# Kernel optimization log

Measured on AMD Instinct MI355X. Metric: run time of the kernel, lower is better.

Reference implementation:

```python
import jax, jax.numpy as jnp
import numpy as np

N_HEADS = 8
N_POINTS = 4
SPATIAL = np.array([[64, 64], [32, 32], [16, 16], [8, 8]], dtype=np.int32)


def setup_inputs() -> dict:
    key = jax.random.key(0)
    ks = jax.random.split(key, 12)
    d = 256
    H, L, P, N = N_HEADS, SPATIAL.shape[0], N_POINTS, 8
    lens = SPATIAL[:, 0] * SPATIAL[:, 1]
    Lin = int(lens.sum())
    Lq = Lin
    query = jax.random.normal(ks[0], (N, Lq, d), jnp.float32)
    reference_points = jax.random.uniform(ks[1], (N, Lq, L, 2), jnp.float32)
    input_flatten = jax.random.normal(ks[2], (N, Lin, d), jnp.float32)
    input_spatial_shapes = jnp.asarray(SPATIAL)
    starts = np.concatenate([[0], np.cumsum(lens)[:-1]]).astype(np.int32)
    input_level_start_index = jnp.asarray(starts)
    s = 1.0 / np.sqrt(d)
    W_off = jax.random.normal(ks[3], (H * L * P * 2, d), jnp.float32) * 0.01
    b_off = jax.random.normal(ks[4], (H * L * P * 2,), jnp.float32) * 0.5
    W_attn = jax.random.normal(ks[5], (H * L * P, d), jnp.float32) * 0.02
    b_attn = jnp.zeros((H * L * P,), jnp.float32)
    W_val = jax.random.normal(ks[6], (d, d), jnp.float32) * s
    b_val = jnp.zeros((d,), jnp.float32)
    W_out = jax.random.normal(ks[7], (d, d), jnp.float32) * s
    b_out = jnp.zeros((d,), jnp.float32)
    return {
        'query': query, 'reference_points': reference_points,
        'input_flatten': input_flatten,
        'input_spatial_shapes': input_spatial_shapes,
        'input_level_start_index': input_level_start_index,
        'W_off': W_off, 'b_off': b_off, 'W_attn': W_attn, 'b_attn': b_attn,
        'W_val': W_val, 'b_val': b_val, 'W_out': W_out, 'b_out': b_out,
    }


def _bilinear(img, Hl, Wl, x, y):
    # img: [B, Ch, Hl*Wl]; x, y: [B, Q, P] pixel coords (align_corners=False)
    # zero padding mode: out-of-range corners contribute 0
    x0 = jnp.floor(x)
    y0 = jnp.floor(y)
    wx = x - x0
    wy = y - y0

    def gather(xi, yi):
        valid = (xi >= 0) & (xi <= Wl - 1) & (yi >= 0) & (yi <= Hl - 1)
        ii = jnp.clip(xi, 0, Wl - 1).astype(jnp.int32)
        jj = jnp.clip(yi, 0, Hl - 1).astype(jnp.int32)
        idx = jj * Wl + ii  # [B, Q, P]
        B, Q, P = idx.shape
        v = jnp.take_along_axis(img, idx.reshape(B, 1, Q * P), axis=2)
        v = v.reshape(B, img.shape[1], Q, P)
        return v * valid[:, None].astype(img.dtype)

    return (gather(x0, y0) * ((1 - wx) * (1 - wy))[:, None]
            + gather(x0 + 1, y0) * (wx * (1 - wy))[:, None]
            + gather(x0, y0 + 1) * ((1 - wx) * wy)[:, None]
            + gather(x0 + 1, y0 + 1) * (wx * wy)[:, None])


def reference(query, reference_points, input_flatten, input_spatial_shapes,
              input_level_start_index, W_off, b_off, W_attn, b_attn,
              W_val, b_val, W_out, b_out):
    shapes = np.asarray(input_spatial_shapes)  # static structural metadata
    N, Lq, d = query.shape
    Lin = input_flatten.shape[1]
    L = shapes.shape[0]
    H, P = N_HEADS, N_POINTS
    Ch = d // H

    value = input_flatten @ W_val.T + b_val                       # [N, Lin, d]
    value = value.reshape(N, Lin, H, Ch).transpose(0, 2, 3, 1)    # [N, H, Ch, Lin]
    value = value.reshape(N * H, Ch, Lin)

    off = (query @ W_off.T + b_off).reshape(N, Lq, H, L, P, 2)
    attn = (query @ W_attn.T + b_attn).reshape(N, Lq, H, L * P)
    attn = jax.nn.softmax(attn, axis=-1).reshape(N, Lq, H, L, P)

    # normalizer is (W, H) per level
    norm = jnp.asarray(np.stack([shapes[:, 1], shapes[:, 0]], -1), query.dtype)
    loc = reference_points[:, :, None, :, None, :] + off / norm[None, None, None, :, None, :]

    attn_p = attn.transpose(0, 2, 1, 3, 4).reshape(N * H, Lq, L, P)
    starts = np.concatenate([[0], np.cumsum(shapes[:, 0] * shapes[:, 1])])

    out = jnp.zeros((N * H, Ch, Lq), query.dtype)
    for l in range(L):
        Hl, Wl = int(shapes[l, 0]), int(shapes[l, 1])
        v_l = value[:, :, starts[l]:starts[l + 1]]                # [B, Ch, Hl*Wl]
        g = loc[:, :, :, l].transpose(0, 2, 1, 3, 4).reshape(N * H, Lq, P, 2)
        # grid_sample align_corners=False with grid=2*loc-1 -> pixel = loc*W - 0.5
        x = g[..., 0] * Wl - 0.5
        y = g[..., 1] * Hl - 0.5
        samp = _bilinear(v_l, Hl, Wl, x, y)                       # [B, Ch, Lq, P]
        out = out + jnp.einsum('bcqp,bqp->bcq', samp, attn_p[:, :, l])

    out = out.reshape(N, H, Ch, Lq).transpose(0, 3, 1, 2).reshape(N, Lq, d)
    return out @ W_out.T + b_out
```

## Files before the change

### kernel.cpp

```cpp
#include <hip/hip_runtime.h>
#include <hip/hip_bf16.h>
#include <hip/hip_fp16.h>

#define NQ   5440
#define NB   8
#define DIM  256
#define NH   8
#define CHN  32
#define NLV  4
#define NPT  4
#define MTOT (NB * NQ)

typedef __attribute__((ext_vector_type(8))) short s16x8;
typedef __attribute__((ext_vector_type(4))) float f32x4;
typedef unsigned short ushort_t;
typedef unsigned int uint_t;

#define WVAL 0
#define WOFF 65536
#define WATT 131072
#define WOUT 163840
#define WTOT 229376

__device__ __forceinline__ short f2bf(float x) {
    union { __hip_bfloat16 b; short s; } u;
    u.b = __float2bfloat16(x);
    return u.s;
}

__device__ __forceinline__ void gload_lds16(const void* g, void* l) {
    __builtin_amdgcn_global_load_lds(
        (const __attribute__((address_space(1))) unsigned int*)g,
        (__attribute__((address_space(3))) unsigned int*)l, 16, 0, 0);
}

__device__ __forceinline__ void cvt8b(const float* s, ushort_t* d) {
    f32x4 a = *(const f32x4*)s, b = *(const f32x4*)(s + 4);
    s16x8 v;
#pragma unroll
    for (int e = 0; e < 4; ++e) { v[e] = f2bf(a[e]); v[e + 4] = f2bf(b[e]); }
    *(s16x8*)d = v;
}

__global__ __launch_bounds__(256) void cvt_weights(const float* __restrict__ wv,
                                                   const float* __restrict__ wo,
                                                   const float* __restrict__ wa,
                                                   const float* __restrict__ wu,
                                                   ushort_t* __restrict__ wb) {
    const int i = (blockIdx.x * 256 + threadIdx.x) * 8;
    if (i >= WTOT) return;
    const float* src;
    int off;
    if (i < WOFF)      { src = wv; off = WVAL; }
    else if (i < WATT) { src = wo; off = WOFF; }
    else if (i < WOUT) { src = wa; off = WATT; }
    else               { src = wu; off = WOUT; }
    cvt8b(src + (i - off), wb + i);
}

__device__ __forceinline__ void stC(float* p, float v) { *p = v; }
__device__ __forceinline__ void stC(__half* p, float v) { *p = __float2half(v); }
__device__ __forceinline__ void stC(ushort_t* p, float v) { *(short*)p = f2bf(v); }

template <typename AT, typename CT>
__device__ __forceinline__ void gemm_core(const AT* __restrict__ A,
                                          const ushort_t* __restrict__ Wt,
                                          const float* __restrict__ biasT,
                                          CT* __restrict__ Ct, int ldC, int rowBase) {
    __shared__ ushort_t As[128 * 64];
    __shared__ ushort_t Ws[128 * 64];

    const int t = threadIdx.x;
    const int lane = t & 63, w = t >> 6;
    const int wm = w >> 1, wn = w & 1;
    const int lr = lane & 15, quad = lane >> 4;

    f32x4 acc[4][4];
#pragma unroll
    for (int i = 0; i < 4; ++i)
#pragma unroll
        for (int j = 0; j < 4; ++j)
#pragma unroll
            for (int r = 0; r < 4; ++r) acc[i][j][r] = 0.f;

    for (int ks = 0; ks < 4; ++ks) {
        if (ks) __syncthreads();
#pragma unroll
        for (int i = 0; i < 4; ++i) {
            const int c = t + i * 256;
            const int r = c >> 3, s = c & 7;
            const int g = (s - r) & 7;
            const int ke = ks * 64 + g * 8;
            gload_lds16(Wt + (size_t)r * DIM + ke,
                        &Ws[(size_t)(i * 256 + w * 64) * 8]);
            if constexpr (sizeof(AT) == 2) {
                gload_lds16(A + (size_t)(rowBase + r) * DIM + ke,
                            &As[(size_t)(i * 256 + w * 64) * 8]);
            } else {
                const float* pa = (const float*)A + (size_t)(rowBase + r) * DIM + ke;
                f32x4 a0 = *(const f32x4*)pa, a1 = *(const f32x4*)(pa + 4);
                s16x8 av;
#pragma unroll
                for (int e = 0; e < 4; ++e) {
                    av[e] = f2bf(a0[e]);
                    av[e + 4] = f2bf(a1[e]);
                }
                *(s16x8*)&As[(size_t)c * 8] = av;
            }
        }
        __syncthreads();
#pragma unroll
        for (int kk = 0; kk < 64; kk += 32) {
            s16x8 afr[4], wfr[4];
            const int G = (kk >> 3) + quad;
#pragma unroll
            for (int i = 0; i < 4; ++i) {
                const int R = wm * 64 + i * 16 + lr;
                afr[i] = *(const s16x8*)&As[(R * 8 + ((G + R) & 7)) * 8];
            }
#pragma unroll
            for (int j = 0; j < 4; ++j) {
                const int R = wn * 64 + j * 16 + lr;
                wfr[j] = *(const s16x8*)&Ws[(R * 8 + ((G + R) & 7)) * 8];
            }
#pragma unroll
            for (int i = 0; i < 4; ++i)
#pragma unroll
                for (int j = 0; j < 4; ++j)
                    acc[i][j] = __builtin_amdgcn_mfma_f32_16x16x32_bf16(
                        afr[i], wfr[j], acc[i][j], 0, 0, 0);
        }
    }

    float bj[4];
#pragma unroll
    for (int j = 0; j < 4; ++j) bj[j] = biasT[wn * 64 + j * 16 + lr];
#pragma unroll
    for (int i = 0; i < 4; ++i)
#pragma unroll
        for (int r = 0; r < 4; ++r) {
            int row = rowBase + wm * 64 + i * 16 + quad * 4 + r;
#pragma unroll
            for (int j = 0; j < 4; ++j) {
                int col = wn * 64 + j * 16 + lr;
                stC(&Ct[(size_t)row * ldC + col], acc[i][j][r] + bj[j]);
            }
        }
}

__global__ __launch_bounds__(256) void gemm_fused(const float* __restrict__ inputf,
                                                  const float* __restrict__ query,
                                                  const ushort_t* __restrict__ wb,
                                                  const float* __restrict__ b_val,
                                                  const float* __restrict__ b_off,
                                                  const float* __restrict__ b_attn,
                                                  __half* __restrict__ bval,
                                                  __half* __restrict__ v_off,
                                                  __half* __restrict__ v_attn) {
    const int gy = blockIdx.y;
    const int rowBase = blockIdx.x * 128;
    if (gy < 2)
        gemm_core<float, __half>(inputf, wb + WVAL + (size_t)gy * 128 * DIM,
                                 b_val + gy * 128, bval + gy * 128, DIM, rowBase);
    else if (gy < 4)
        gemm_core<float, __half>(query, wb + WOFF + (size_t)(gy - 2) * 128 * DIM,
                                 b_off + (gy - 2) * 128, v_off + (gy - 2) * 128, DIM,
                                 rowBase);
    else
        gemm_core<float, __half>(query, wb + WATT, b_attn, v_attn, 128, rowBase);
}

__global__ __launch_bounds__(256) void gemm_out(const ushort_t* __restrict__ A,
                                                const ushort_t* __restrict__ wb,
                                                const float* __restrict__ bias,
                                                float* __restrict__ C) {
    gemm_core<ushort_t, float>(A, wb + WOUT + (size_t)blockIdx.y * 128 * DIM,
                               bias + blockIdx.y * 128, C + blockIdx.y * 128, DIM,
                               blockIdx.x * 128);
}

__global__ __launch_bounds__(256, 8) void sample_kernel(
    const float* __restrict__ refp,
    const __half* __restrict__ off,
    const __half* __restrict__ attn,
    const __half* __restrict__ bval,
    const int* __restrict__ shapes,
    const int* __restrict__ starts,
    ushort_t* __restrict__ sampb)
{
    const int n = blockIdx.x & 7;
    const int qBase = n * NQ + (blockIdx.x >> 3) * 8;
    const int t = threadIdx.x;

    __shared__ __align__(16) uint4 sitem[1024];

#pragma unroll
    for (int it = 0; it < 4; ++it) {
        const int i = t + it * 256;
        const int q8 = i >> 7, hlp = i & 127;
        const int h = hlp >> 4, lp = hlp & 15, l = lp >> 2;
        const int q = qBase + q8;
        const int Wl = shapes[2 * l + 1], Hl = shapes[2 * l];
        const float Wf = (float)Wl, Hf = (float)Hl;
        const float2 rp = *(const float2*)(refp + ((size_t)q * NLV + l) * 2);
        const __half2 oo2 = ((const __half2*)off)[(size_t)q * 128 + h * 16 + lp];
        const float2 oo = __half22float2(oo2);
        const float x = (rp.x + oo.x / Wf) * Wf - 0.5f;
        const float y = (rp.y + oo.y / Hf) * Hf - 0.5f;

        float logit = __half2float(attn[(size_t)q * 128 + h * 16 + lp]);
        float m = logit;
#pragma unroll
        for (int s = 8; s >= 1; s >>= 1) m = fmaxf(m, __shfl_xor(m, s, 16));
        float e = __expf(logit - m);
        float ss = e;
#pragma unroll
        for (int s = 8; s >= 1; s >>= 1) ss += __shfl_xor(ss, s, 16);
        const float aw = e / ss;

        const float xf = floorf(x), yf = floorf(y);
        const int ix = (int)xf, iy = (int)yf;
        const float wx = x - xf, wy = y - yf;
        const int ix1 = ix + 1, iy1 = iy + 1;
        const bool bx0 = (ix >= 0) & (ix < Wl);
        const bool bx1 = (ix1 >= 0) & (ix1 < Wl);
        const bool by0 = (iy >= 0) & (iy < Hl);
        const bool by1 = (iy1 >= 0) & (iy1 < Hl);
        const int cx0 = min(max(ix, 0), Wl - 1), cx1 = min(max(ix1, 0), Wl - 1);
        const int cy0 = min(max(iy, 0), Hl - 1), cy1 = min(max(iy1, 0), Hl - 1);
        const int base = n * NQ + starts[l];

        uint4 item;
        item.x = (uint_t)(base + cy0 * Wl + cx0) << 9;
        const uint_t dx  = (uint_t)(cx1 - cx0) << 9;
        const uint_t dyW = (uint_t)((cy1 - cy0) * Wl) << 9;
        item.y = dx | (dyW << 16);
        union { __half2 h; uint_t u; } p01, p23;
        p01.h = __halves2half2(
            __float2half((bx0 && by0) ? aw * (1.f - wx) * (1.f - wy) : 0.f),
            __float2half((bx1 && by0) ? aw * wx * (1.f - wy) : 0.f));
        p23.h = __halves2half2(
            __float2half((bx0 && by1) ? aw * (1.f - wx) * wy : 0.f),
            __float2half((bx1 && by1) ? aw * wx * wy : 0.f));
        item.z = p01.u;
        item.w = p23.u;
        sitem[i] = item;
    }
    __syncthreads();

    const int q8 = t >> 5, r = t & 31;
    const int h = r >> 2, cg = r & 3;
    const int q = qBase + q8;
    const char* vb = (const char*)bval + h * 64 + cg * 16;
    const int slotBase = (q8 << 7) + (h << 4);

    __half2 acch[4];
    float accf[8];
#pragma unroll
    for (int e = 0; e < 4; ++e) acch[e] = __float2half2_rn(0.f);
#pragma unroll
    for (int e = 0; e < 8; ++e) accf[e] = 0.f;

#pragma unroll
    for (int j = 0; j < 16; ++j) {
        const int lp = (j + h) & 15;
        const uint4 itv = sitem[slotBase + lp];
        const uint_t a00 = itv.x;
        const uint_t dx = itv.y & 0xffffu, dyW = itv.y >> 16;
        uint_t ad[4];
        ad[0] = a00;
        ad[1] = a00 + dx;
        ad[2] = a00 + dyW;
        ad[3] = a00 + dx + dyW;
        union { uint_t u; __half2 h; } w01, w23;
        w01.u = itv.z; w23.u = itv.w;
        __half2 wc[4];
        wc[0] = __half2half2(__low2half(w01.h));
        wc[1] = __half2half2(__high2half(w01.h));
        wc[2] = __half2half2(__low2half(w23.h));
        wc[3] = __half2half2(__high2half(w23.h));

        uint4 u[4];
#pragma unroll
        for (int c = 0; c < 4; ++c)
            u[c] = *(const uint4*)(vb + (size_t)ad[c]);
#pragma unroll
        for (int c = 0; c < 4; ++c) {
            const __half2* hv = (const __half2*)&u[c];
#pragma unroll
            for (int e = 0; e < 4; ++e) acch[e] = __hfma2(hv[e], wc[c], acch[e]);
        }
        if ((j & 3) == 3) {
#pragma unroll
            for (int e = 0; e < 4; ++e) {
                float2 f = __half22float2(acch[e]);
                accf[2 * e] += f.x;
                accf[2 * e + 1] += f.y;
                acch[e] = __float2half2_rn(0.f);
            }
        }
    }

    s16x8 o;
#pragma unroll
    for (int e = 0; e < 8; ++e) o[e] = f2bf(accf[e]);
    *(s16x8*)(sampb + (size_t)q * DIM + h * CHN + cg * 8) = o;
}

extern "C" void kernel_launch(void* const* d_in, const int* in_sizes, int n_in,
                              void* d_out, int out_size, void* d_ws, size_t ws_size,
                              hipStream_t stream) {
    const float* query  = (const float*)d_in[0];
    const float* refp   = (const float*)d_in[1];
    const float* inputf = (const float*)d_in[2];
    const int* shapes   = (const int*)d_in[3];
    const int* starts   = (const int*)d_in[4];
    const float* W_off  = (const float*)d_in[5];
    const float* b_off  = (const float*)d_in[6];
    const float* W_attn = (const float*)d_in[7];
    const float* b_attn = (const float*)d_in[8];
    const float* W_val  = (const float*)d_in[9];
    const float* b_val  = (const float*)d_in[10];
    const float* W_out  = (const float*)d_in[11];
    const float* b_out  = (const float*)d_in[12];
    float* out = (float*)d_out;

    const size_t AB = (size_t)MTOT * DIM * 2;
    char* ws = (char*)d_ws;
    ushort_t* wb     = (ushort_t*)ws;
    __half*   bval   = (__half*)(ws + 512 * 1024);
    __half*   v_off  = (__half*)(ws + 512 * 1024 + AB);
    __half*   v_attn = (__half*)(ws + 512 * 1024 + 2 * AB);
    ushort_t* sampb  = (ushort_t*)(ws + 512 * 1024 + 2 * AB + AB / 2);

    cvt_weights<<<dim3(WTOT / 2048), dim3(256), 0, stream>>>(W_val, W_off, W_attn,
                                                             W_out, wb);
    gemm_fused<<<dim3(MTOT / 128, 5), dim3(256), 0, stream>>>(
        inputf, query, wb, b_val, b_off, b_attn, bval, v_off, v_attn);
    sample_kernel<<<dim3(MTOT / 8), dim3(256), 0, stream>>>(
        refp, v_off, v_attn, bval, shapes, starts, sampb);
    gemm_out<<<dim3(MTOT / 128, 2), dim3(256), 0, stream>>>(sampb, wb, b_out, out);
}
```

Before: 275.9 us.

## Fuse deformable sampling with output projection GEMM in one kernel

```diff
diff --git a/kernel.cpp b/kernel.cpp
--- a/kernel.cpp
+++ b/kernel.cpp
@@ -58,15 +58,11 @@
     cvt8b(src + (i - off), wb + i);
 }
 
-__device__ __forceinline__ void stC(float* p, float v) { *p = v; }
-__device__ __forceinline__ void stC(__half* p, float v) { *p = __float2half(v); }
-__device__ __forceinline__ void stC(ushort_t* p, float v) { *(short*)p = f2bf(v); }
-
-template <typename AT, typename CT>
-__device__ __forceinline__ void gemm_core(const AT* __restrict__ A,
-                                          const ushort_t* __restrict__ Wt,
-                                          const float* __restrict__ biasT,
-                                          CT* __restrict__ Ct, int ldC, int rowBase) {
+__device__ __forceinline__ void gemm_core_f32(const float* __restrict__ A,
+                                              const ushort_t* __restrict__ Wt,
+                                              const float* __restrict__ biasT,
+                                              __half* __restrict__ Ct, int ldC,
+                                              int rowBase) {
     __shared__ ushort_t As[128 * 64];
     __shared__ ushort_t Ws[128 * 64];
 
@@ -88,25 +84,20 @@
 #pragma unroll
         for (int i = 0; i < 4; ++i) {
             const int c = t + i * 256;
-            const int r = c >> 3, s = c & 7;
-            const int g = (s - r) & 7;
+            const int r = c >> 3, s2 = c & 7;
+            const int g = (s2 - r) & 7;
             const int ke = ks * 64 + g * 8;
             gload_lds16(Wt + (size_t)r * DIM + ke,
                         &Ws[(size_t)(i * 256 + w * 64) * 8]);
-            if constexpr (sizeof(AT) == 2) {
-                gload_lds16(A + (size_t)(rowBase + r) * DIM + ke,
-                            &As[(size_t)(i * 256 + w * 64) * 8]);
-            } else {
-                const float* pa = (const float*)A + (size_t)(rowBase + r) * DIM + ke;
-                f32x4 a0 = *(const f32x4*)pa, a1 = *(const f32x4*)(pa + 4);
-                s16x8 av;
-#pragma unroll
-                for (int e = 0; e < 4; ++e) {
-                    av[e] = f2bf(a0[e]);
-                    av[e + 4] = f2bf(a1[e]);
-                }
-                *(s16x8*)&As[(size_t)c * 8] = av;
-            }
+            const float* pa = A + (size_t)(rowBase + r) * DIM + ke;
+            f32x4 a0 = *(const f32x4*)pa, a1 = *(const f32x4*)(pa + 4);
+            s16x8 av;
+#pragma unroll
+            for (int e = 0; e < 4; ++e) {
+                av[e] = f2bf(a0[e]);
+                av[e + 4] = f2bf(a1[e]);
+            }
+            *(s16x8*)&As[(size_t)c * 8] = av;
         }
         __syncthreads();
 #pragma unroll
@@ -143,7 +134,7 @@
 #pragma unroll
             for (int j = 0; j < 4; ++j) {
                 int col = wn * 64 + j * 16 + lr;
-                stC(&Ct[(size_t)row * ldC + col], acc[i][j][r] + bj[j]);
+                Ct[(size_t)row * ldC + col] = __float2half(acc[i][j][r] + bj[j]);
             }
         }
 }
@@ -160,151 +151,219 @@
     const int gy = blockIdx.y;
     const int rowBase = blockIdx.x * 128;
     if (gy < 2)
-        gemm_core<float, __half>(inputf, wb + WVAL + (size_t)gy * 128 * DIM,
-                                 b_val + gy * 128, bval + gy * 128, DIM, rowBase);
+        gemm_core_f32(inputf, wb + WVAL + (size_t)gy * 128 * DIM,
+                      b_val + gy * 128, bval + gy * 128, DIM, rowBase);
     else if (gy < 4)
-        gemm_core<float, __half>(query, wb + WOFF + (size_t)(gy - 2) * 128 * DIM,
-                                 b_off + (gy - 2) * 128, v_off + (gy - 2) * 128, DIM,
-                                 rowBase);
+        gemm_core_f32(query, wb + WOFF + (size_t)(gy - 2) * 128 * DIM,
+                      b_off + (gy - 2) * 128, v_off + (gy - 2) * 128, DIM, rowBase);
     else
-        gemm_core<float, __half>(query, wb + WATT, b_attn, v_attn, 128, rowBase);
-}
-
-__global__ __launch_bounds__(256) void gemm_out(const ushort_t* __restrict__ A,
-                                                const ushort_t* __restrict__ wb,
-                                                const float* __restrict__ bias,
-                                                float* __restrict__ C) {
-    gemm_core<ushort_t, float>(A, wb + WOUT + (size_t)blockIdx.y * 128 * DIM,
-                               bias + blockIdx.y * 128, C + blockIdx.y * 128, DIM,
-                               blockIdx.x * 128);
-}
-
-__global__ __launch_bounds__(256, 8) void sample_kernel(
+        gemm_core_f32(query, wb + WATT, b_attn, v_attn, 128, rowBase);
+}
+
+__global__ __launch_bounds__(256) void sample_out(
     const float* __restrict__ refp,
     const __half* __restrict__ off,
     const __half* __restrict__ attn,
     const __half* __restrict__ bval,
     const int* __restrict__ shapes,
     const int* __restrict__ starts,
-    ushort_t* __restrict__ sampb)
+    const ushort_t* __restrict__ wb,
+    const float* __restrict__ b_out,
+    float* __restrict__ out)
 {
+    __shared__ __align__(16) char smem[49152];
+    ushort_t* samp = (ushort_t*)smem;
+    ushort_t* Ws   = (ushort_t*)(smem + 32768);
+    uint4*  scratch = (uint4*)(smem + 32768);
+
     const int n = blockIdx.x & 7;
-    const int qBase = n * NQ + (blockIdx.x >> 3) * 8;
+    const int pan = blockIdx.x >> 3;
     const int t = threadIdx.x;
-
-    __shared__ __align__(16) uint4 sitem[1024];
-
-#pragma unroll
-    for (int it = 0; it < 4; ++it) {
-        const int i = t + it * 256;
-        const int q8 = i >> 7, hlp = i & 127;
-        const int h = hlp >> 4, lp = hlp & 15, l = lp >> 2;
-        const int q = qBase + q8;
-        const int Wl = shapes[2 * l + 1], Hl = shapes[2 * l];
-        const float Wf = (float)Wl, Hf = (float)Hl;
-        const float2 rp = *(const float2*)(refp + ((size_t)q * NLV + l) * 2);
-        const __half2 oo2 = ((const __half2*)off)[(size_t)q * 128 + h * 16 + lp];
-        const float2 oo = __half22float2(oo2);
-        const float x = (rp.x + oo.x / Wf) * Wf - 0.5f;
-        const float y = (rp.y + oo.y / Hf) * Hf - 0.5f;
-
-        float logit = __half2float(attn[(size_t)q * 128 + h * 16 + lp]);
-        float m = logit;
-#pragma unroll
-        for (int s = 8; s >= 1; s >>= 1) m = fmaxf(m, __shfl_xor(m, s, 16));
-        float e = __expf(logit - m);
-        float ss = e;
-#pragma unroll
-        for (int s = 8; s >= 1; s >>= 1) ss += __shfl_xor(ss, s, 16);
-        const float aw = e / ss;
-
-        const float xf = floorf(x), yf = floorf(y);
-        const int ix = (int)xf, iy = (int)yf;
-        const float wx = x - xf, wy = y - yf;
-        const int ix1 = ix + 1, iy1 = iy + 1;
-        const bool bx0 = (ix >= 0) & (ix < Wl);
-        const bool bx1 = (ix1 >= 0) & (ix1 < Wl);
-        const bool by0 = (iy >= 0) & (iy < Hl);
-        const bool by1 = (iy1 >= 0) & (iy1 < Hl);
-        const int cx0 = min(max(ix, 0), Wl - 1), cx1 = min(max(ix1, 0), Wl - 1);
-        const int cy0 = min(max(iy, 0), Hl - 1), cy1 = min(max(iy1, 0), Hl - 1);
-        const int base = n * NQ + starts[l];
-
-        uint4 item;
-        item.x = (uint_t)(base + cy0 * Wl + cx0) << 9;
-        const uint_t dx  = (uint_t)(cx1 - cx0) << 9;
-        const uint_t dyW = (uint_t)((cy1 - cy0) * Wl) << 9;
-        item.y = dx | (dyW << 16);
-        union { __half2 h; uint_t u; } p01, p23;
-        p01.h = __halves2half2(
-            __float2half((bx0 && by0) ? aw * (1.f - wx) * (1.f - wy) : 0.f),
-            __float2half((bx1 && by0) ? aw * wx * (1.f - wy) : 0.f));
-        p23.h = __halves2half2(
-            __float2half((bx0 && by1) ? aw * (1.f - wx) * wy : 0.f),
-            __float2half((bx1 && by1) ? aw * wx * wy : 0.f));
-        item.z = p01.u;
-        item.w = p23.u;
-        sitem[i] = item;
+    const int tl = t & 127, sub = t >> 7;
+
+    for (int it8 = 0; it8 < 8; ++it8) {
+        const int qBase = n * NQ + pan * 64 + it8 * 8 + sub * 4;
+        __syncthreads();
+#pragma unroll
+        for (int it = 0; it < 4; ++it) {
+            const int i = tl + it * 128;
+            const int q4 = i >> 7, hlp = i & 127;
+            const int h = hlp >> 4, lp = hlp & 15, l = lp >> 2;
+            const int q = qBase + q4;
+            const int Wl = shapes[2 * l + 1], Hl = shapes[2 * l];
+            const float Wf = (float)Wl, Hf = (float)Hl;
+            const float2 rp = *(const float2*)(refp + ((size_t)q * NLV + l) * 2);
+            const __half2 oo2 = ((const __half2*)off)[(size_t)q * 128 + h * 16 + lp];
+            const float2 oo = __half22float2(oo2);
+            const float x = (rp.x + oo.x / Wf) * Wf - 0.5f;
+            const float y = (rp.y + oo.y / Hf) * Hf - 0.5f;
+
+            float logit = __half2float(attn[(size_t)q * 128 + h * 16 + lp]);
+            float m = logit;
+#pragma unroll
+            for (int s = 8; s >= 1; s >>= 1) m = fmaxf(m, __shfl_xor(m, s, 16));
+            float e = __expf(logit - m);
+            float ss = e;
+#pragma unroll
+            for (int s = 8; s >= 1; s >>= 1) ss += __shfl_xor(ss, s, 16);
+            const float aw = e / ss;
+
+            const float xf = floorf(x), yf = floorf(y);
+            const int ix = (int)xf, iy = (int)yf;
+            const float wx = x - xf, wy = y - yf;
+            const int ix1 = ix + 1, iy1 = iy + 1;
+            const bool bx0 = (ix >= 0) & (ix < Wl);
+            const bool bx1 = (ix1 >= 0) & (ix1 < Wl);
+            const bool by0 = (iy >= 0) & (iy < Hl);
+            const bool by1 = (iy1 >= 0) & (iy1 < Hl);
+            const int cx0 = min(max(ix, 0), Wl - 1), cx1 = min(max(ix1, 0), Wl - 1);
+            const int cy0 = min(max(iy, 0), Hl - 1), cy1 = min(max(iy1, 0), Hl - 1);
+            const int base = n * NQ + starts[l];
+
+            uint4 item;
+            item.x = (uint_t)(base + cy0 * Wl + cx0) << 9;
+            const uint_t dx  = (uint_t)(cx1 - cx0) << 9;
+            const uint_t dyW = (uint_t)((cy1 - cy0) * Wl) << 9;
+            item.y = dx | (dyW << 16);
+            union { __half2 h; uint_t u; } p01, p23;
+            p01.h = __halves2half2(
+                __float2half((bx0 && by0) ? aw * (1.f - wx) * (1.f - wy) : 0.f),
+                __float2half((bx1 && by0) ? aw * wx * (1.f - wy) : 0.f));
+            p23.h = __halves2half2(
+                __float2half((bx0 && by1) ? aw * (1.f - wx) * wy : 0.f),
+                __float2half((bx1 && by1) ? aw * wx * wy : 0.f));
+            item.z = p01.u;
+            item.w = p23.u;
+            scratch[sub * 512 + i] = item;
+        }
+        __syncthreads();
+
+        const int q4 = tl >> 5, r = tl & 31;
+        const int h = r >> 2, cg = r & 3;
+        const char* vb = (const char*)bval + h * 64 + cg * 16;
+        const int slotBase = sub * 512 + (q4 << 7) + (h << 4);
+
+        __half2 acch[4];
+        float accf[8];
+#pragma unroll
+        for (int e = 0; e < 4; ++e) acch[e] = __float2half2_rn(0.f);
+#pragma unroll
+        for (int e = 0; e < 8; ++e) accf[e] = 0.f;
+
+#pragma unroll
+        for (int j = 0; j < 16; ++j) {
+            const int lp = (j + h) & 15;
+            const uint4 itv = scratch[slotBase + lp];
+            const uint_t a00 = itv.x;
+            const uint_t dx = itv.y & 0xffffu, dyW = itv.y >> 16;
+            uint_t ad[4];
+            ad[0] = a00;
+            ad[1] = a00 + dx;
+            ad[2] = a00 + dyW;
+            ad[3] = a00 + dx + dyW;
+            union { uint_t u; __half2 h; } w01, w23;
+            w01.u = itv.z; w23.u = itv.w;
+            __half2 wc[4];
+            wc[0] = __half2half2(__low2half(w01.h));
+            wc[1] = __half2half2(__high2half(w01.h));
+            wc[2] = __half2half2(__low2half(w23.h));
+            wc[3] = __half2half2(__high2half(w23.h));
+
+            uint4 u[4];
+#pragma unroll
+            for (int c = 0; c < 4; ++c)
+                u[c] = *(const uint4*)(vb + (size_t)ad[c]);
+#pragma unroll
+            for (int c = 0; c < 4; ++c) {
+                const __half2* hv = (const __half2*)&u[c];
+#pragma unroll
+                for (int e = 0; e < 4; ++e) acch[e] = __hfma2(hv[e], wc[c], acch[e]);
+            }
+            if ((j & 3) == 3) {
+#pragma unroll
+                for (int e = 0; e < 4; ++e) {
+                    float2 f = __half22float2(acch[e]);
+                    accf[2 * e] += f.x;
+                    accf[2 * e + 1] += f.y;
+                    acch[e] = __float2half2_rn(0.f);
+                }
+            }
+        }
+
+        s16x8 o;
+#pragma unroll
+        for (int e = 0; e < 8; ++e) o[e] = f2bf(accf[e]);
+        const int row = it8 * 8 + sub * 4 + q4;
+        const int cs = (h * 4 + cg) ^ (row & 7);
+        *(s16x8*)&samp[row * 256 + cs * 8] = o;
     }
-    __syncthreads();
-
-    const int q8 = t >> 5, r = t & 31;
-    const int h = r >> 2, cg = r & 3;
-    const int q = qBase + q8;
-    const char* vb = (const char*)bval + h * 64 + cg * 16;
-    const int slotBase = (q8 << 7) + (h << 4);
-
-    __half2 acch[4];
-    float accf[8];
-#pragma unroll
-    for (int e = 0; e < 4; ++e) acch[e] = __float2half2_rn(0.f);
-#pragma unroll
-    for (int e = 0; e < 8; ++e) accf[e] = 0.f;
-
-#pragma unroll
-    for (int j = 0; j < 16; ++j) {
-        const int lp = (j + h) & 15;
-        const uint4 itv = sitem[slotBase + lp];
-        const uint_t a00 = itv.x;
-        const uint_t dx = itv.y & 0xffffu, dyW = itv.y >> 16;
-        uint_t ad[4];
-        ad[0] = a00;
-        ad[1] = a00 + dx;
-        ad[2] = a00 + dyW;
-        ad[3] = a00 + dx + dyW;
-        union { uint_t u; __half2 h; } w01, w23;
-        w01.u = itv.z; w23.u = itv.w;
-        __half2 wc[4];
-        wc[0] = __half2half2(__low2half(w01.h));
-        wc[1] = __half2half2(__high2half(w01.h));
-        wc[2] = __half2half2(__low2half(w23.h));
-        wc[3] = __half2half2(__high2half(w23.h));
-
-        uint4 u[4];
-#pragma unroll
-        for (int c = 0; c < 4; ++c)
-            u[c] = *(const uint4*)(vb + (size_t)ad[c]);
-#pragma unroll
-        for (int c = 0; c < 4; ++c) {
-            const __half2* hv = (const __half2*)&u[c];
-#pragma unroll
-            for (int e = 0; e < 4; ++e) acch[e] = __hfma2(hv[e], wc[c], acch[e]);
-        }
-        if ((j & 3) == 3) {
-#pragma unroll
-            for (int e = 0; e < 4; ++e) {
-                float2 f = __half22float2(acch[e]);
-                accf[2 * e] += f.x;
-                accf[2 * e + 1] += f.y;
-                acch[e] = __float2half2_rn(0.f);
-            }
-        }
+
+    const int lane = t & 63, w = t >> 6;
+    const int wm = w >> 1, wn = w & 1;
+    const int lr = lane & 15, quad = lane >> 4;
+
+#pragma unroll 1
+    for (int jn = 0; jn < 2; ++jn) {
+        const ushort_t* Wt = wb + WOUT + (size_t)jn * 128 * DIM;
+        f32x4 acc[2][4];
+#pragma unroll
+        for (int i = 0; i < 2; ++i)
+#pragma unroll
+            for (int j = 0; j < 4; ++j)
+#pragma unroll
+                for (int rr = 0; rr < 4; ++rr) acc[i][j][rr] = 0.f;
+
+        for (int ks = 0; ks < 4; ++ks) {
+            __syncthreads();
+#pragma unroll
+            for (int i = 0; i < 4; ++i) {
+                const int c = t + i * 256;
+                const int rw = c >> 3, s2 = c & 7;
+                const int g = (s2 - rw) & 7;
+                const int ke = ks * 64 + g * 8;
+                gload_lds16(Wt + (size_t)rw * DIM + ke,
+                            &Ws[(size_t)(i * 256 + w * 64) * 8]);
+            }
+            __syncthreads();
+#pragma unroll
+            for (int kk = 0; kk < 64; kk += 32) {
+                s16x8 afr[2], wfr[4];
+                const int G = (kk >> 3) + quad;
+#pragma unroll
+                for (int i = 0; i < 2; ++i) {
+                    const int R = wm * 32 + i * 16 + lr;
+                    const int kc = ks * 8 + G;
+                    afr[i] = *(const s16x8*)&samp[R * 256 + (kc ^ (R & 7)) * 8];
+                }
+#pragma unroll
+                for (int j = 0; j < 4; ++j) {
+                    const int R = wn * 64 + j * 16 + lr;
+                    wfr[j] = *(const s16x8*)&Ws[(R * 8 + ((G + R) & 7)) * 8];
+                }
+#pragma unroll
+                for (int i = 0; i < 2; ++i)
+#pragma unroll
+                    for (int j = 0; j < 4; ++j)
+                        acc[i][j] = __builtin_amdgcn_mfma_f32_16x16x32_bf16(
+                            afr[i], wfr[j], acc[i][j], 0, 0, 0);
+            }
+        }
+
+        float bj[4];
+#pragma unroll
+        for (int j = 0; j < 4; ++j) bj[j] = b_out[jn * 128 + wn * 64 + j * 16 + lr];
+#pragma unroll
+        for (int i = 0; i < 2; ++i)
+#pragma unroll
+            for (int rr = 0; rr < 4; ++rr) {
+                const int q = n * NQ + pan * 64 + wm * 32 + i * 16 + quad * 4 + rr;
+#pragma unroll
+                for (int j = 0; j < 4; ++j) {
+                    const int col = jn * 128 + wn * 64 + j * 16 + lr;
+                    out[(size_t)q * DIM + col] = acc[i][j][rr] + bj[j];
+                }
+            }
     }
-
-    s16x8 o;
-#pragma unroll
-    for (int e = 0; e < 8; ++e) o[e] = f2bf(accf[e]);
-    *(s16x8*)(sampb + (size_t)q * DIM + h * CHN + cg * 8) = o;
 }
 
 extern "C" void kernel_launch(void* const* d_in, const int* in_sizes, int n_in,
@@ -331,13 +390,11 @@
     __half*   bval   = (__half*)(ws + 512 * 1024);
     __half*   v_off  = (__half*)(ws + 512 * 1024 + AB);
     __half*   v_attn = (__half*)(ws + 512 * 1024 + 2 * AB);
-    ushort_t* sampb  = (ushort_t*)(ws + 512 * 1024 + 2 * AB + AB / 2);
 
     cvt_weights<<<dim3(WTOT / 2048), dim3(256), 0, stream>>>(W_val, W_off, W_attn,
                                                              W_out, wb);
     gemm_fused<<<dim3(MTOT / 128, 5), dim3(256), 0, stream>>>(
         inputf, query, wb, b_val, b_off, b_attn, bval, v_off, v_attn);
-    sample_kernel<<<dim3(MTOT / 8), dim3(256), 0, stream>>>(
-        refp, v_off, v_attn, bval, shapes, starts, sampb);
-    gemm_out<<<dim3(MTOT / 128, 2), dim3(256), 0, stream>>>(sampb, wb, b_out, out);
-}
+    sample_out<<<dim3(MTOT / 64), dim3(256), 0, stream>>>(
+        refp, v_off, v_attn, bval, shapes, starts, wb, b_out, out);
+}
```

Measured after the change: 284.8 us. 3.3% more time.
